# Optimization experiments

Hardware: AMD Instinct MI355X
Metric: run time of the kernel (lower is better)

## Reference

```python
import jax, jax.numpy as jnp
import numpy as np
import math

B, H, L, D = 2, 16, 2048, 64


def setup_inputs() -> dict:
    key = jax.random.key(0)
    kq, kk, kv, km, kb = jax.random.split(key, 5)
    Q = jax.random.normal(kq, (B, H, L, D), dtype=jnp.float32)
    K = jax.random.normal(kk, (B, H, L, D), dtype=jnp.float32)
    V = jax.random.normal(kv, (B, H, L, D), dtype=jnp.float32)
    mask = jax.random.randint(km, (B, 1, L, L), 0, 2, dtype=jnp.int32)
    attn_bias = jax.random.normal(kb, (1, H, L, L), dtype=jnp.float32)
    return {"Q": Q, "K": K, "V": V, "mask": mask, "attn_bias": attn_bias,
            "last_layer_flag": 0}


def reference(Q, K, V, mask, attn_bias, last_layer_flag):
    d_tensor = K.shape[-1]
    # score: [B, H, L, L] = Q @ K^T / sqrt(d)
    score = jnp.einsum("bhqd,bhkd->bhqk", Q, K) / math.sqrt(d_tensor)
    if mask is not None:
        score = jnp.where(mask == 0, jnp.float32(-10000.0), score)
    if attn_bias is not None:
        score = score + attn_bias
    if last_layer_flag:
        return jnp.mean(score, axis=1)  # mean over heads: [B, L, L]
    score = jax.nn.softmax(score, axis=-1)
    out = jnp.einsum("bhqk,bhkd->bhqd", score, V)  # [B, H, L, D]
    return (out, score)
```

## Files before the change

### kernel.cpp

```cpp
#include <hip/hip_runtime.h>
#include <hip/hip_bf16.h>

#define Bb 2
#define Hh 16
#define Ll 2048
#define Dd 64
#define OUT_ELEMS (Bb*Hh*Ll*Dd)
#define BHL (Bb*Hh*Ll)
#define NT (Ll/64)

typedef __attribute__((ext_vector_type(8))) short bf16x8;
typedef __attribute__((ext_vector_type(4))) float f32x4;
typedef __attribute__((ext_vector_type(4))) int i32x4;
typedef __attribute__((ext_vector_type(2))) unsigned int u32x2;

__device__ __forceinline__ unsigned int pk2(float a, float b) {
    unsigned int r;
    asm("v_cvt_pk_bf16_f32 %0, %1, %2" : "=v"(r) : "v"(a), "v"(b));
    return r;
}
__device__ __forceinline__ float bf2f(short s) {
    union { float f; unsigned u; } c;
    c.u = ((unsigned)(unsigned short)s) << 16;
    return c.f;
}
__device__ __forceinline__ void bar() {
    asm volatile("s_waitcnt lgkmcnt(0)" ::: "memory");
    __builtin_amdgcn_s_barrier();
}
__device__ __forceinline__ int swz(int row, int colByte) {
    return row * 128 + (colByte ^ ((row & 7) << 4));
}

__global__ __launch_bounds__(256)
void attn_exp(const float* __restrict__ Q, const float* __restrict__ K,
              const int* __restrict__ M, const float* __restrict__ Bi,
              float* __restrict__ ws)
{
    __shared__ char Ks[2][64 * 128];
    __shared__ char Ps[64 * 128];

    const int bid = blockIdx.x;
    const int ks = bid & 3;
    const int b  = (bid >> 2) & 1;
    const int qt = (bid >> 3) & 31;
    const int h  = bid >> 8;
    const int q0 = qt * 64;
    const int kb = ks * 512;

    const int tid  = threadIdx.x;
    const int w    = tid >> 6;
    const int lane = tid & 63;
    const int g    = lane >> 4;
    const int c16  = lane & 15;
    const int qr   = w * 16 + c16;

    const float* Qp = Q + ((size_t)(b * Hh + h) * Ll + q0) * Dd;
    const float* Kp = K + (size_t)(b * Hh + h) * Ll * Dd;
    const int*   mrow = M  + (size_t)b * Ll * Ll + ((size_t)q0 + qr) * Ll;
    const float* brow = Bi + (size_t)h * Ll * Ll + ((size_t)q0 + qr) * Ll;
    unsigned short* srow = (unsigned short*)(ws + 4 * (size_t)BHL)
                         + ((size_t)(b * Hh + h) * Ll + q0 + qr) * (size_t)Ll;

    bf16x8 qf[2];
    {
        const float* qrow = Qp + qr * Dd;
#pragma unroll
        for (int kk = 0; kk < 2; ++kk) {
            f32x4 a = *(const f32x4*)(qrow + kk * 32 + g * 8);
            f32x4 c = *(const f32x4*)(qrow + kk * 32 + g * 8 + 4);
            union { bf16x8 v; unsigned int u[4]; } cvt;
            cvt.u[0] = pk2(a[0], a[1]); cvt.u[1] = pk2(a[2], a[3]);
            cvt.u[2] = pk2(c[0], c[1]); cvt.u[3] = pk2(c[2], c[3]);
            qf[kk] = cvt.v;
        }
    }

    float4 kreg[4];
    i32x4  m4[4];
    f32x4  b4[4];
    const int r0 = tid >> 4, d0 = (tid & 15) * 4;

    auto issueK = [&](int k0) {
#pragma unroll
        for (int rep = 0; rep < 4; ++rep)
            kreg[rep] = *(const float4*)(Kp + (size_t)(k0 + r0 + rep * 16) * Dd + d0);
    };
    auto writeK = [&](char* buf) {
#pragma unroll
        for (int rep = 0; rep < 4; ++rep) {
            u32x2 u = { pk2(kreg[rep].x, kreg[rep].y), pk2(kreg[rep].z, kreg[rep].w) };
            *(u32x2*)(buf + swz(r0 + rep * 16, d0 * 2)) = u;
        }
    };
    auto issueMB = [&](int k0) {
#pragma unroll
        for (int ct = 0; ct < 4; ++ct) {
            m4[ct] = *(const i32x4*)(mrow + k0 + ct * 16 + g * 4);
            b4[ct] = *(const f32x4*)(brow + k0 + ct * 16 + g * 4);
        }
    };

    issueK(kb);
    issueMB(kb);
    writeK(Ks[0]);
    issueK(kb + 64);
    bar();

    float rsv[4] = {0.f, 0.f, 0.f, 0.f};
    for (int t = 0; t < 8; ++t) {
        f32x4 sacc[4] = {{0,0,0,0},{0,0,0,0},{0,0,0,0},{0,0,0,0}};
        __builtin_amdgcn_s_setprio(1);
#pragma unroll
        for (int kk = 0; kk < 2; ++kk)
#pragma unroll
            for (int ct = 0; ct < 4; ++ct) {
                bf16x8 af = *(const bf16x8*)(Ks[t & 1] + swz(ct * 16 + c16, kk * 64 + g * 16));
                sacc[ct] = __builtin_amdgcn_mfma_f32_16x16x32_bf16(af, qf[kk], sacc[ct], 0, 0, 0);
            }
        __builtin_amdgcn_s_setprio(0);
#pragma unroll
        for (int ct = 0; ct < 4; ++ct) {
            f32x4 e;
#pragma unroll
            for (int r = 0; r < 4; ++r) {
                float s = m4[ct][r] == 0 ? -10000.0f
                                         : fmaf(sacc[ct][r], 0.125f, b4[ct][r]);
                e[r] = __expf(s);
                rsv[ct] += e[r];
            }
            u32x2 u = { pk2(e[0], e[1]), pk2(e[2], e[3]) };
            *(u32x2*)(Ps + swz(qr, ct * 32 + g * 8)) = u;
        }
        const int kc = kb + t * 64;
#pragma unroll
        for (int half = 0; half < 2; ++half) {
            bf16x8 d = *(const bf16x8*)(Ps + swz(qr, half * 64 + g * 16));
            *(bf16x8*)(srow + kc + half * 32 + g * 8) = d;
        }
        writeK(Ks[(t + 1) & 1]);
        issueK(kb + ((t + 2) & 7) * 64);
        issueMB(kb + ((t + 1) & 7) * 64);
        bar();
    }
    float rs = (rsv[0] + rsv[1]) + (rsv[2] + rsv[3]);
    rs += __shfl_xor(rs, 16);
    rs += __shfl_xor(rs, 32);
    if (g == 0)
        ws[(size_t)ks * BHL + (size_t)(b * Hh + h) * Ll + q0 + qr] = rs;
}

__global__ __launch_bounds__(256)
void attn_pv2(const float* __restrict__ V, const float* __restrict__ ws,
              float* __restrict__ out)
{
    __shared__ char VTs[2][64 * 128];

    const int bid = blockIdx.x;
    const int ks = bid & 3;
    const int b  = (bid >> 2) & 1;
    const int qt = (bid >> 3) & 31;
    const int h  = bid >> 8;
    const int q0 = qt * 64;
    const int kb = ks * 512;
    const int NTB = 8;

    const int tid  = threadIdx.x;
    const int w    = tid >> 6;
    const int lane = tid & 63;
    const int g    = lane >> 4;
    const int c16  = lane & 15;
    const int qr   = w * 16 + c16;

    const float* Vp = V + (size_t)(b * Hh + h) * Ll * Dd;
    float* Op = out + ((size_t)(b * Hh + h) * Ll + q0) * Dd;
    float* prow = out + OUT_ELEMS + ((size_t)(b * Hh + h) * Ll + q0 + qr) * (size_t)Ll;
    const unsigned short* srow = (const unsigned short*)(ws + 4 * (size_t)BHL)
                               + ((size_t)(b * Hh + h) * Ll + q0 + qr) * (size_t)Ll;

    float inv, invO[4];
    {
        size_t idx = (size_t)(b * Hh + h) * Ll + q0 + qr;
        float s = ws[idx] + ws[(size_t)BHL + idx]
                + ws[2 * (size_t)BHL + idx] + ws[3 * (size_t)BHL + idx];
        inv = 1.0f / s;
#pragma unroll
        for (int r = 0; r < 4; ++r) invO[r] = __shfl(inv, g * 4 + r);
    }

    float vreg[16];
    auto issueV = [&](int k0) {
#pragma unroll
        for (int r = 0; r < 4; ++r)
#pragma unroll
            for (int i = 0; i < 4; ++i)
                vreg[r * 4 + i] = Vp[(size_t)(k0 + w * 16 + r * 4 + i) * Dd + lane];
    };
    auto writeV = [&](char* buf) {
#pragma unroll
        for (int r = 0; r < 4; ++r) {
            u32x2 u = { pk2(vreg[r * 4 + 0], vreg[r * 4 + 1]),
                        pk2(vreg[r * 4 + 2], vreg[r * 4 + 3]) };
            *(u32x2*)(buf + swz(lane, (w * 16 + r * 4) * 2)) = u;
        }
    };

    bf16x8 pa[2];
    auto loadA = [&](int t) {
        pa[0] = *(const bf16x8*)(srow + kb + t * 64 + g * 8);
        pa[1] = *(const bf16x8*)(srow + kb + t * 64 + 32 + g * 8);
    };

    issueV(kb);
    loadA(0);
    writeV(VTs[0]);
    issueV(kb + 64);
    bar();

    f32x4 oacc[4] = {{0,0,0,0},{0,0,0,0},{0,0,0,0},{0,0,0,0}};
    for (int t = 0; t < NTB; ++t) {
        __builtin_amdgcn_s_setprio(1);
#pragma unroll
        for (int kk = 0; kk < 2; ++kk)
#pragma unroll
            for (int dt = 0; dt < 4; ++dt) {
                bf16x8 vf = *(const bf16x8*)(VTs[t & 1] + swz(dt * 16 + c16, kk * 64 + g * 16));
                oacc[dt] = __builtin_amdgcn_mfma_f32_16x16x32_bf16(pa[kk], vf, oacc[dt], 0, 0, 0);
            }
        __builtin_amdgcn_s_setprio(0);
        const int k0 = kb + t * 64;
#pragma unroll
        for (int kk = 0; kk < 2; ++kk) {
            f32x4 p0, p1;
#pragma unroll
            for (int j = 0; j < 4; ++j) {
                p0[j] = bf2f(pa[kk][j]) * inv;
                p1[j] = bf2f(pa[kk][4 + j]) * inv;
            }
            __builtin_nontemporal_store(p0, (f32x4*)(prow + k0 + kk * 32 + g * 8));
            __builtin_nontemporal_store(p1, (f32x4*)(prow + k0 + kk * 32 + g * 8 + 4));
        }
        loadA((t + 1) & 7);
        writeV(VTs[(t + 1) & 1]);
        issueV(kb + ((t + 2) & 7) * 64);
        bar();
    }
#pragma unroll
    for (int dt = 0; dt < 4; ++dt)
#pragma unroll
        for (int r = 0; r < 4; ++r)
            unsafeAtomicAdd(&Op[(w * 16 + g * 4 + r) * Dd + dt * 16 + c16],
                            oacc[dt][r] * invO[r]);
}

extern "C" void kernel_launch(void* const* d_in, const int* in_sizes, int n_in,
                              void* d_out, int out_size, void* d_ws, size_t ws_size,
                              hipStream_t stream) {
    const float* Q  = (const float*)d_in[0];
    const float* K  = (const float*)d_in[1];
    const float* V  = (const float*)d_in[2];
    const int*   M  = (const int*)d_in[3];
    const float* Bi = (const float*)d_in[4];
    float* out = (float*)d_out;
    float* ws  = (float*)d_ws;

    const size_t need = 4ull * BHL * sizeof(float)
                      + (size_t)BHL * Ll * sizeof(unsigned short);
    if (ws_size >= need) {
        (void)hipMemsetAsync(out, 0, (size_t)OUT_ELEMS * sizeof(float), stream);
        attn_exp<<<dim3(4096), dim3(256), 0, stream>>>(Q, K, M, Bi, ws);
        attn_pv2<<<dim3(4096), dim3(256), 0, stream>>>(V, ws, out);
    }
}
```

Baseline: 449.4 us.

## Fuse PV product into exp kernel, store split-K O partials in output scratch

```diff
diff --git a/kernel.cpp b/kernel.cpp
--- a/kernel.cpp
+++ b/kernel.cpp
@@ -7,7 +7,6 @@
 #define Dd 64
 #define OUT_ELEMS (Bb*Hh*Ll*Dd)
 #define BHL (Bb*Hh*Ll)
-#define NT (Ll/64)
 
 typedef __attribute__((ext_vector_type(8))) short bf16x8;
 typedef __attribute__((ext_vector_type(4))) float f32x4;
@@ -33,11 +32,13 @@
 }
 
 __global__ __launch_bounds__(256)
-void attn_exp(const float* __restrict__ Q, const float* __restrict__ K,
-              const int* __restrict__ M, const float* __restrict__ Bi,
-              float* __restrict__ ws)
+void attn_main(const float* __restrict__ Q, const float* __restrict__ K,
+               const float* __restrict__ V, const int* __restrict__ M,
+               const float* __restrict__ Bi, float* __restrict__ ws,
+               float* __restrict__ out)
 {
     __shared__ char Ks[2][64 * 128];
+    __shared__ char VTs[2][64 * 128];
     __shared__ char Ps[64 * 128];
 
     const int bid = blockIdx.x;
@@ -57,10 +58,13 @@
 
     const float* Qp = Q + ((size_t)(b * Hh + h) * Ll + q0) * Dd;
     const float* Kp = K + (size_t)(b * Hh + h) * Ll * Dd;
+    const float* Vp = V + (size_t)(b * Hh + h) * Ll * Dd;
     const int*   mrow = M  + (size_t)b * Ll * Ll + ((size_t)q0 + qr) * Ll;
     const float* brow = Bi + (size_t)h * Ll * Ll + ((size_t)q0 + qr) * Ll;
     unsigned short* srow = (unsigned short*)(ws + 4 * (size_t)BHL)
                          + ((size_t)(b * Hh + h) * Ll + q0 + qr) * (size_t)Ll;
+    float* op = out + OUT_ELEMS + (size_t)ks * OUT_ELEMS
+              + ((size_t)(b * Hh + h) * Ll + q0) * Dd;
 
     bf16x8 qf[2];
     {
@@ -77,6 +81,7 @@
     }
 
     float4 kreg[4];
+    float  vreg[16];
     i32x4  m4[4];
     f32x4  b4[4];
     const int r0 = tid >> 4, d0 = (tid & 15) * 4;
@@ -93,6 +98,21 @@
             *(u32x2*)(buf + swz(r0 + rep * 16, d0 * 2)) = u;
         }
     };
+    auto issueV = [&](int k0) {
+#pragma unroll
+        for (int r = 0; r < 4; ++r)
+#pragma unroll
+            for (int i = 0; i < 4; ++i)
+                vreg[r * 4 + i] = Vp[(size_t)(k0 + w * 16 + r * 4 + i) * Dd + lane];
+    };
+    auto writeV = [&](char* buf) {
+#pragma unroll
+        for (int r = 0; r < 4; ++r) {
+            u32x2 u = { pk2(vreg[r * 4 + 0], vreg[r * 4 + 1]),
+                        pk2(vreg[r * 4 + 2], vreg[r * 4 + 3]) };
+            *(u32x2*)(buf + swz(lane, (w * 16 + r * 4) * 2)) = u;
+        }
+    };
     auto issueMB = [&](int k0) {
 #pragma unroll
         for (int ct = 0; ct < 4; ++ct) {
@@ -103,11 +123,15 @@
 
     issueK(kb);
     issueMB(kb);
+    issueV(kb);
     writeK(Ks[0]);
+    writeV(VTs[0]);
     issueK(kb + 64);
+    issueV(kb + 64);
     bar();
 
     float rsv[4] = {0.f, 0.f, 0.f, 0.f};
+    f32x4 oacc[4] = {{0,0,0,0},{0,0,0,0},{0,0,0,0},{0,0,0,0}};
     for (int t = 0; t < 8; ++t) {
         f32x4 sacc[4] = {{0,0,0,0},{0,0,0,0},{0,0,0,0},{0,0,0,0}};
         __builtin_amdgcn_s_setprio(1);
@@ -133,13 +157,22 @@
             *(u32x2*)(Ps + swz(qr, ct * 32 + g * 8)) = u;
         }
         const int kc = kb + t * 64;
-#pragma unroll
-        for (int half = 0; half < 2; ++half) {
-            bf16x8 d = *(const bf16x8*)(Ps + swz(qr, half * 64 + g * 16));
-            *(bf16x8*)(srow + kc + half * 32 + g * 8) = d;
-        }
+        __builtin_amdgcn_s_setprio(1);
+#pragma unroll
+        for (int kk = 0; kk < 2; ++kk) {
+            bf16x8 pa = *(const bf16x8*)(Ps + swz(qr, kk * 64 + g * 16));
+            *(bf16x8*)(srow + kc + kk * 32 + g * 8) = pa;
+#pragma unroll
+            for (int dt = 0; dt < 4; ++dt) {
+                bf16x8 vf = *(const bf16x8*)(VTs[t & 1] + swz(dt * 16 + c16, kk * 64 + g * 16));
+                oacc[dt] = __builtin_amdgcn_mfma_f32_16x16x32_bf16(pa, vf, oacc[dt], 0, 0, 0);
+            }
+        }
+        __builtin_amdgcn_s_setprio(0);
         writeK(Ks[(t + 1) & 1]);
+        writeV(VTs[(t + 1) & 1]);
         issueK(kb + ((t + 2) & 7) * 64);
+        issueV(kb + ((t + 2) & 7) * 64);
         issueMB(kb + ((t + 1) & 7) * 64);
         bar();
     }
@@ -148,109 +181,49 @@
     rs += __shfl_xor(rs, 32);
     if (g == 0)
         ws[(size_t)ks * BHL + (size_t)(b * Hh + h) * Ll + q0 + qr] = rs;
+#pragma unroll
+    for (int dt = 0; dt < 4; ++dt)
+#pragma unroll
+        for (int r = 0; r < 4; ++r)
+            op[(w * 16 + g * 4 + r) * Dd + dt * 16 + c16] = oacc[dt][r];
 }
 
 __global__ __launch_bounds__(256)
-void attn_pv2(const float* __restrict__ V, const float* __restrict__ ws,
-              float* __restrict__ out)
+void norm_o(const float* __restrict__ ws, float* __restrict__ out)
 {
-    __shared__ char VTs[2][64 * 128];
-
-    const int bid = blockIdx.x;
-    const int ks = bid & 3;
-    const int b  = (bid >> 2) & 1;
-    const int qt = (bid >> 3) & 31;
-    const int h  = bid >> 8;
-    const int q0 = qt * 64;
-    const int kb = ks * 512;
-    const int NTB = 8;
-
-    const int tid  = threadIdx.x;
-    const int w    = tid >> 6;
-    const int lane = tid & 63;
-    const int g    = lane >> 4;
-    const int c16  = lane & 15;
-    const int qr   = w * 16 + c16;
-
-    const float* Vp = V + (size_t)(b * Hh + h) * Ll * Dd;
-    float* Op = out + ((size_t)(b * Hh + h) * Ll + q0) * Dd;
-    float* prow = out + OUT_ELEMS + ((size_t)(b * Hh + h) * Ll + q0 + qr) * (size_t)Ll;
-    const unsigned short* srow = (const unsigned short*)(ws + 4 * (size_t)BHL)
-                               + ((size_t)(b * Hh + h) * Ll + q0 + qr) * (size_t)Ll;
-
-    float inv, invO[4];
-    {
-        size_t idx = (size_t)(b * Hh + h) * Ll + q0 + qr;
-        float s = ws[idx] + ws[(size_t)BHL + idx]
-                + ws[2 * (size_t)BHL + idx] + ws[3 * (size_t)BHL + idx];
-        inv = 1.0f / s;
-#pragma unroll
-        for (int r = 0; r < 4; ++r) invO[r] = __shfl(inv, g * 4 + r);
-    }
-
-    float vreg[16];
-    auto issueV = [&](int k0) {
-#pragma unroll
-        for (int r = 0; r < 4; ++r)
-#pragma unroll
-            for (int i = 0; i < 4; ++i)
-                vreg[r * 4 + i] = Vp[(size_t)(k0 + w * 16 + r * 4 + i) * Dd + lane];
-    };
-    auto writeV = [&](char* buf) {
-#pragma unroll
-        for (int r = 0; r < 4; ++r) {
-            u32x2 u = { pk2(vreg[r * 4 + 0], vreg[r * 4 + 1]),
-                        pk2(vreg[r * 4 + 2], vreg[r * 4 + 3]) };
-            *(u32x2*)(buf + swz(lane, (w * 16 + r * 4) * 2)) = u;
-        }
-    };
-
-    bf16x8 pa[2];
-    auto loadA = [&](int t) {
-        pa[0] = *(const bf16x8*)(srow + kb + t * 64 + g * 8);
-        pa[1] = *(const bf16x8*)(srow + kb + t * 64 + 32 + g * 8);
-    };
-
-    issueV(kb);
-    loadA(0);
-    writeV(VTs[0]);
-    issueV(kb + 64);
-    bar();
-
-    f32x4 oacc[4] = {{0,0,0,0},{0,0,0,0},{0,0,0,0},{0,0,0,0}};
-    for (int t = 0; t < NTB; ++t) {
-        __builtin_amdgcn_s_setprio(1);
-#pragma unroll
-        for (int kk = 0; kk < 2; ++kk)
-#pragma unroll
-            for (int dt = 0; dt < 4; ++dt) {
-                bf16x8 vf = *(const bf16x8*)(VTs[t & 1] + swz(dt * 16 + c16, kk * 64 + g * 16));
-                oacc[dt] = __builtin_amdgcn_mfma_f32_16x16x32_bf16(pa[kk], vf, oacc[dt], 0, 0, 0);
-            }
-        __builtin_amdgcn_s_setprio(0);
-        const int k0 = kb + t * 64;
-#pragma unroll
-        for (int kk = 0; kk < 2; ++kk) {
-            f32x4 p0, p1;
-#pragma unroll
-            for (int j = 0; j < 4; ++j) {
-                p0[j] = bf2f(pa[kk][j]) * inv;
-                p1[j] = bf2f(pa[kk][4 + j]) * inv;
-            }
-            __builtin_nontemporal_store(p0, (f32x4*)(prow + k0 + kk * 32 + g * 8));
-            __builtin_nontemporal_store(p1, (f32x4*)(prow + k0 + kk * 32 + g * 8 + 4));
-        }
-        loadA((t + 1) & 7);
-        writeV(VTs[(t + 1) & 1]);
-        issueV(kb + ((t + 2) & 7) * 64);
-        bar();
-    }
-#pragma unroll
-    for (int dt = 0; dt < 4; ++dt)
-#pragma unroll
-        for (int r = 0; r < 4; ++r)
-            unsafeAtomicAdd(&Op[(w * 16 + g * 4 + r) * Dd + dt * 16 + c16],
-                            oacc[dt][r] * invO[r]);
+    const size_t idx = ((size_t)blockIdx.x * 256 + threadIdx.x) * 4;
+    const size_t row = idx >> 6;
+    float s = ws[row] + ws[(size_t)BHL + row]
+            + ws[2 * (size_t)BHL + row] + ws[3 * (size_t)BHL + row];
+    const float inv = 1.0f / s;
+    const float* Opart = out + OUT_ELEMS;
+    f32x4 o = *(const f32x4*)(Opart + idx);
+    o += *(const f32x4*)(Opart + (size_t)OUT_ELEMS + idx);
+    o += *(const f32x4*)(Opart + 2 * (size_t)OUT_ELEMS + idx);
+    o += *(const f32x4*)(Opart + 3 * (size_t)OUT_ELEMS + idx);
+    o *= inv;
+    *(f32x4*)(out + idx) = o;
+}
+
+__global__ __launch_bounds__(256)
+void norm_p(const float* __restrict__ ws, float* __restrict__ out)
+{
+    const size_t i = ((size_t)blockIdx.x * 256 + threadIdx.x) * 8;
+    const size_t row = i >> 11;
+    float s = ws[row] + ws[(size_t)BHL + row]
+            + ws[2 * (size_t)BHL + row] + ws[3 * (size_t)BHL + row];
+    const float inv = 1.0f / s;
+    const unsigned short* Ex = (const unsigned short*)(ws + 4 * (size_t)BHL);
+    bf16x8 e = *(const bf16x8*)(Ex + i);
+    f32x4 p0, p1;
+#pragma unroll
+    for (int j = 0; j < 4; ++j) {
+        p0[j] = bf2f(e[j]) * inv;
+        p1[j] = bf2f(e[4 + j]) * inv;
+    }
+    float* dst = out + OUT_ELEMS + i;
+    __builtin_nontemporal_store(p0, (f32x4*)(dst));
+    __builtin_nontemporal_store(p1, (f32x4*)(dst + 4));
 }
 
 extern "C" void kernel_launch(void* const* d_in, const int* in_sizes, int n_in,
@@ -267,8 +240,8 @@
     const size_t need = 4ull * BHL * sizeof(float)
                       + (size_t)BHL * Ll * sizeof(unsigned short);
     if (ws_size >= need) {
-        (void)hipMemsetAsync(out, 0, (size_t)OUT_ELEMS * sizeof(float), stream);
-        attn_exp<<<dim3(4096), dim3(256), 0, stream>>>(Q, K, M, Bi, ws);
-        attn_pv2<<<dim3(4096), dim3(256), 0, stream>>>(V, ws, out);
-    }
-}
+        attn_main<<<dim3(4096),  dim3(256), 0, stream>>>(Q, K, V, M, Bi, ws, out);
+        norm_o  <<<dim3(OUT_ELEMS / 1024), dim3(256), 0, stream>>>(ws, out);
+        norm_p  <<<dim3((size_t)BHL * Ll / 2048), dim3(256), 0, stream>>>(ws, out);
+    }
+}
```

Result: slower. 494.6 us (+10.1%).

## Store exp scratch in tiled layout and stage probability writes through LDS

Applied to the files above, without the earlier changes.

```diff
diff --git a/kernel.cpp b/kernel.cpp
--- a/kernel.cpp
+++ b/kernel.cpp
@@ -7,9 +7,10 @@
 #define Dd 64
 #define OUT_ELEMS (Bb*Hh*Ll*Dd)
 #define BHL (Bb*Hh*Ll)
-#define NT (Ll/64)
+#define TILE 4096
 
 typedef __attribute__((ext_vector_type(8))) short bf16x8;
+typedef __attribute__((ext_vector_type(4))) short bf16x4;
 typedef __attribute__((ext_vector_type(4))) float f32x4;
 typedef __attribute__((ext_vector_type(4))) int i32x4;
 typedef __attribute__((ext_vector_type(2))) unsigned int u32x2;
@@ -59,8 +60,8 @@
     const float* Kp = K + (size_t)(b * Hh + h) * Ll * Dd;
     const int*   mrow = M  + (size_t)b * Ll * Ll + ((size_t)q0 + qr) * Ll;
     const float* brow = Bi + (size_t)h * Ll * Ll + ((size_t)q0 + qr) * Ll;
-    unsigned short* srow = (unsigned short*)(ws + 4 * (size_t)BHL)
-                         + ((size_t)(b * Hh + h) * Ll + q0 + qr) * (size_t)Ll;
+    unsigned short* Exg = (unsigned short*)(ws + 4 * (size_t)BHL);
+    const size_t tb0 = (((size_t)(b * Hh + h) * 32 + qt) * 32 + (kb >> 6)) * TILE;
 
     bf16x8 qf[2];
     {
@@ -132,11 +133,13 @@
             u32x2 u = { pk2(e[0], e[1]), pk2(e[2], e[3]) };
             *(u32x2*)(Ps + swz(qr, ct * 32 + g * 8)) = u;
         }
-        const int kc = kb + t * 64;
-#pragma unroll
-        for (int half = 0; half < 2; ++half) {
-            bf16x8 d = *(const bf16x8*)(Ps + swz(qr, half * 64 + g * 16));
-            *(bf16x8*)(srow + kc + half * 32 + g * 8) = d;
+        {
+            unsigned short* tp = Exg + tb0 + (size_t)t * TILE + qr * 64;
+#pragma unroll
+            for (int half = 0; half < 2; ++half) {
+                bf16x8 d = *(const bf16x8*)(Ps + swz(qr, half * 64 + g * 16));
+                *(bf16x8*)(tp + half * 32 + g * 8) = d;
+            }
         }
         writeK(Ks[(t + 1) & 1]);
         issueK(kb + ((t + 2) & 7) * 64);
@@ -155,6 +158,7 @@
               float* __restrict__ out)
 {
     __shared__ char VTs[2][64 * 128];
+    __shared__ char Pst[64 * 512];
 
     const int bid = blockIdx.x;
     const int ks = bid & 3;
@@ -163,7 +167,6 @@
     const int h  = bid >> 8;
     const int q0 = qt * 64;
     const int kb = ks * 512;
-    const int NTB = 8;
 
     const int tid  = threadIdx.x;
     const int w    = tid >> 6;
@@ -174,9 +177,9 @@
 
     const float* Vp = V + (size_t)(b * Hh + h) * Ll * Dd;
     float* Op = out + ((size_t)(b * Hh + h) * Ll + q0) * Dd;
-    float* prow = out + OUT_ELEMS + ((size_t)(b * Hh + h) * Ll + q0 + qr) * (size_t)Ll;
-    const unsigned short* srow = (const unsigned short*)(ws + 4 * (size_t)BHL)
-                               + ((size_t)(b * Hh + h) * Ll + q0 + qr) * (size_t)Ll;
+    float* Pout = out + OUT_ELEMS + (size_t)(b * Hh + h) * Ll * Ll;
+    const unsigned short* Exg = (const unsigned short*)(ws + 4 * (size_t)BHL);
+    const size_t tb0 = (((size_t)(b * Hh + h) * 32 + qt) * 32 + (kb >> 6)) * TILE;
 
     float inv, invO[4];
     {
@@ -207,8 +210,9 @@
 
     bf16x8 pa[2];
     auto loadA = [&](int t) {
-        pa[0] = *(const bf16x8*)(srow + kb + t * 64 + g * 8);
-        pa[1] = *(const bf16x8*)(srow + kb + t * 64 + 32 + g * 8);
+        const unsigned short* tp = Exg + tb0 + (size_t)t * TILE + qr * 64;
+        pa[0] = *(const bf16x8*)(tp + g * 8);
+        pa[1] = *(const bf16x8*)(tp + 32 + g * 8);
     };
 
     issueV(kb);
@@ -218,7 +222,7 @@
     bar();
 
     f32x4 oacc[4] = {{0,0,0,0},{0,0,0,0},{0,0,0,0},{0,0,0,0}};
-    for (int t = 0; t < NTB; ++t) {
+    for (int t = 0; t < 8; ++t) {
         __builtin_amdgcn_s_setprio(1);
 #pragma unroll
         for (int kk = 0; kk < 2; ++kk)
@@ -228,17 +232,25 @@
                 oacc[dt] = __builtin_amdgcn_mfma_f32_16x16x32_bf16(pa[kk], vf, oacc[dt], 0, 0, 0);
             }
         __builtin_amdgcn_s_setprio(0);
-        const int k0 = kb + t * 64;
 #pragma unroll
         for (int kk = 0; kk < 2; ++kk) {
-            f32x4 p0, p1;
-#pragma unroll
-            for (int j = 0; j < 4; ++j) {
-                p0[j] = bf2f(pa[kk][j]) * inv;
-                p1[j] = bf2f(pa[kk][4 + j]) * inv;
-            }
-            __builtin_nontemporal_store(p0, (f32x4*)(prow + k0 + kk * 32 + g * 8));
-            __builtin_nontemporal_store(p1, (f32x4*)(prow + k0 + kk * 32 + g * 8 + 4));
+            int colB = (((t & 3) * 128 + kk * 64 + g * 16)) ^ ((qr & 15) << 4);
+            *(bf16x8*)(Pst + qr * 512 + colB) = pa[kk];
+        }
+        if ((t & 3) == 3) {
+            const int di = t >> 2;
+#pragma unroll
+            for (int i = 0; i < 16; ++i) {
+                const int row = w * 16 + i;
+                const float rinv = __shfl(inv, i);
+                const int colB = (lane * 8) ^ (i << 4);
+                bf16x4 e = *(const bf16x4*)(Pst + row * 512 + colB);
+                f32x4 p;
+#pragma unroll
+                for (int j = 0; j < 4; ++j) p[j] = bf2f(e[j]) * rinv;
+                float* dst = Pout + (size_t)(q0 + row) * Ll + kb + di * 256 + lane * 4;
+                __builtin_nontemporal_store(p, (f32x4*)dst);
+            }
         }
         loadA((t + 1) & 7);
         writeV(VTs[(t + 1) & 1]);
```

Measured after the change: 416.2 us. -7.4%, faster.
